# Optimization experiments

Hardware: AMD Instinct MI355X
Metric: run time of the kernel (lower is better)

## Reference

```python
import jax, jax.numpy as jnp
import numpy as np

D = 1024      # d_model
H = 16        # n_heads
DH = 64       # d_head
K = 4         # conv_kernel
C = H * DH    # channels for depthwise convs


def setup_inputs() -> dict:
    key = jax.random.key(0)
    ks = jax.random.split(key, 16)
    s = 0.02
    w = lambda k, shape: (jax.random.normal(k, shape, jnp.float32) * s)
    return {
        'hidden_states': jax.random.normal(ks[0], (4, 2048, D), jnp.float32),
        'Wq': w(ks[1], (C, D)),
        'Wk': w(ks[2], (C, D)),
        'Wv': w(ks[3], (C, D)),
        'Wa': w(ks[4], (H, D)), 'ba': jnp.zeros((H,), jnp.float32),
        'Wb': w(ks[5], (H, D)), 'bb': jnp.zeros((H,), jnp.float32),
        'conv_q_w': w(ks[6], (C, 1, K)), 'conv_q_b': jnp.zeros((C,), jnp.float32),
        'conv_k_w': w(ks[7], (C, 1, K)), 'conv_k_b': jnp.zeros((C,), jnp.float32),
        'conv_v_w': w(ks[8], (C, 1, K)), 'conv_v_b': jnp.zeros((C,), jnp.float32),
        'Wg': w(ks[9], (C, D)), 'bg': jnp.zeros((C,), jnp.float32),
        'Wo': w(ks[10], (D, C)),
    }


def _causal_conv(x, w, b):
    # x: (B, C, T); depthwise causal conv (torch pads K-1 both sides then slices [:T])
    y = jax.lax.conv_general_dilated(
        x, w, window_strides=(1,), padding=[(K - 1, 0)],
        feature_group_count=C, dimension_numbers=('NCH', 'OIH', 'NCH'))
    return y + b[None, :, None]


def reference(hidden_states, Wq, Wk, Wv, Wa, ba, Wb, bb,
              conv_q_w, conv_q_b, conv_k_w, conv_k_b, conv_v_w, conv_v_b,
              Wg, bg, Wo):
    B, T, _ = hidden_states.shape
    # projections -> (B, C, T) for conv
    q = jnp.einsum('btd,cd->bct', hidden_states, Wq)
    k = jnp.einsum('btd,cd->bct', hidden_states, Wk)
    v = jnp.einsum('btd,cd->bct', hidden_states, Wv)
    q = jax.nn.silu(_causal_conv(q, conv_q_w, conv_q_b))
    k = jax.nn.silu(_causal_conv(k, conv_k_w, conv_k_b))
    v = jax.nn.silu(_causal_conv(v, conv_v_w, conv_v_b))
    # (B, T, H, DH)
    q = q.transpose(0, 2, 1).reshape(B, T, H, DH)
    k = k.transpose(0, 2, 1).reshape(B, T, H, DH)
    v = v.transpose(0, 2, 1).reshape(B, T, H, DH)
    # F.normalize(k, p=2, dim=-1)
    k = k / jnp.maximum(jnp.linalg.norm(k, axis=-1, keepdims=True), 1e-12)
    alpha = jax.nn.sigmoid(jnp.einsum('btd,hd->bth', hidden_states, Wa) + ba)
    beta = jax.nn.sigmoid(jnp.einsum('btd,hd->bth', hidden_states, Wb) + bb)

    def step(S, xs):
        kt, vt, qt, at, bt = xs            # (B,H,DH) x3, (B,H) x2
        v_old = jnp.einsum('bhij,bhj->bhi', S, kt)
        upd = vt - at[..., None] * v_old   # (B,H,DH)
        dS = upd[..., :, None] * kt[..., None, :]
        S = jnp.clip(at[..., None, None] * S + bt[..., None, None] * dS, -5.0, 5.0)
        ot = jnp.einsum('bhij,bhj->bhi', S, qt)
        return S, ot

    S0 = jnp.zeros((B, H, DH, DH), hidden_states.dtype)
    xs = (k.transpose(1, 0, 2, 3), v.transpose(1, 0, 2, 3), q.transpose(1, 0, 2, 3),
          alpha.transpose(1, 0, 2), beta.transpose(1, 0, 2))
    _, ys = jax.lax.scan(step, S0, xs)     # ys: (T, B, H, DH)
    y = ys.transpose(1, 0, 2, 3).reshape(B, T, C)
    g = jax.nn.silu(jnp.einsum('btd,cd->btc', hidden_states, Wg) + bg)
    y = y * g
    out = jnp.einsum('btc,dc->btd', y, Wo)
    return out
```

## Files before the change

### kernel.cpp

```cpp
#include <hip/hip_runtime.h>
#include <cstdint>
#include <cstddef>

#define TSEQ 2048
#define NB   4
#define NH   16
#define MM   (NB * TSEQ)
#define KK   1024
#define NCAT 4224

typedef __attribute__((ext_vector_type(8))) __bf16 bf16x8;
typedef __attribute__((ext_vector_type(4))) float f32x4;
typedef __attribute__((ext_vector_type(4))) int   int4v;

__device__ __forceinline__ unsigned short f2bf(float f) {
  unsigned int u = __float_as_uint(f);
  u += 0x7fffu + ((u >> 16) & 1u);
  return (unsigned short)(u >> 16);
}
__device__ __forceinline__ float bf2f(unsigned short h) {
  return __uint_as_float(((unsigned int)h) << 16);
}
__device__ __forceinline__ float sigmoidf_(float x) { return 1.0f / (1.0f + expf(-x)); }
__device__ __forceinline__ float siluf_(float x)    { return x / (1.0f + expf(-x)); }

__device__ __forceinline__ uint32_t packsplit(float x) {
  unsigned short h = f2bf(x);
  unsigned short l = f2bf(x - bf2f(h));
  return ((uint32_t)h << 16) | (uint32_t)l;
}

union BF8 { bf16x8 v; unsigned short s[8]; };

__device__ __forceinline__ void frag_from_packed(const uint32_t* p, bf16x8& hi, bf16x8& lo) {
  int4v a = *(const int4v*)p;
  int4v b = *(const int4v*)(p + 4);
  BF8 H, L;
#pragma unroll
  for (int e = 0; e < 4; ++e) {
    uint32_t ua = ((const uint32_t*)&a)[e];
    uint32_t ub = ((const uint32_t*)&b)[e];
    H.s[e]     = (unsigned short)(ua >> 16);
    L.s[e]     = (unsigned short)(ua & 0xffffu);
    H.s[e + 4] = (unsigned short)(ub >> 16);
    L.s[e + 4] = (unsigned short)(ub & 0xffffu);
  }
  hi = H.v; lo = L.v;
}

__device__ __forceinline__ f32x4 mfma3(bf16x8 ah, bf16x8 al, bf16x8 bh, bf16x8 bl, f32x4 acc) {
  acc = __builtin_amdgcn_mfma_f32_16x16x32_bf16(ah, bh, acc, 0, 0, 0);
  acc = __builtin_amdgcn_mfma_f32_16x16x32_bf16(ah, bl, acc, 0, 0, 0);
  acc = __builtin_amdgcn_mfma_f32_16x16x32_bf16(al, bh, acc, 0, 0, 0);
  return acc;
}

__global__ void k_split(const float* __restrict__ x, unsigned short* __restrict__ hi,
                        unsigned short* __restrict__ lo, int n) {
  int idx = blockIdx.x * blockDim.x + threadIdx.x;
  if (idx >= n) return;
  float v = x[idx];
  unsigned short h = f2bf(v);
  hi[idx] = h;
  lo[idx] = f2bf(v - bf2f(h));
}

__global__ void k_build_wcat(const float* __restrict__ Wq, const float* __restrict__ Wk,
                             const float* __restrict__ Wv, const float* __restrict__ Wg,
                             const float* __restrict__ Wa, const float* __restrict__ Wb,
                             unsigned short* __restrict__ hi, unsigned short* __restrict__ lo) {
  int idx = blockIdx.x * blockDim.x + threadIdx.x;
  if (idx >= NCAT * KK) return;
  int row = idx >> 10, col = idx & 1023;
  float v = 0.0f;
  if      (row < 1024) v = Wq[idx];
  else if (row < 2048) v = Wk[idx - 1024 * 1024];
  else if (row < 3072) v = Wv[idx - 2048 * 1024];
  else if (row < 4096) v = Wg[idx - 3072 * 1024];
  else if (row < 4112) v = Wa[(row - 4096) * 1024 + col];
  else if (row < 4128) v = Wb[(row - 4112) * 1024 + col];
  unsigned short h = f2bf(v);
  hi[idx] = h;
  lo[idx] = f2bf(v - bf2f(h));
}

__global__ __launch_bounds__(256, 2)
void k_gemm(const unsigned short* __restrict__ Ahi, const unsigned short* __restrict__ Alo,
            const unsigned short* __restrict__ Bhi, const unsigned short* __restrict__ Blo,
            int Kdim, int mode,
            float* __restrict__ Qb, float* __restrict__ Kb, float* __restrict__ Vb,
            float* __restrict__ Gb, float* __restrict__ Ab, float* __restrict__ Bbuf,
            const float* __restrict__ bg, const float* __restrict__ ba, const float* __restrict__ bb,
            float* __restrict__ Out) {
  __shared__ __align__(16) unsigned short As_hi[128 * 32];
  __shared__ __align__(16) unsigned short As_lo[128 * 32];
  __shared__ __align__(16) unsigned short Bs_hi[128 * 32];
  __shared__ __align__(16) unsigned short Bs_lo[128 * 32];

  const int tid  = threadIdx.x;
  const int lane = tid & 63;
  const int l15  = lane & 15;
  const int quad = lane >> 4;
  const int wid  = tid >> 6;
  const int wm   = (wid >> 1) * 64;
  const int wn   = (wid & 1) * 64;
  const int m0   = blockIdx.x * 128;
  const int n0   = blockIdx.y * 128;
  const int srow = tid >> 2;
  const int skc  = (tid & 3) * 8;

  f32x4 acc[4][4];
  f32x4 zero4 = {0.f, 0.f, 0.f, 0.f};
#pragma unroll
  for (int i = 0; i < 4; ++i)
#pragma unroll
    for (int j = 0; j < 4; ++j) acc[i][j] = zero4;

  const unsigned short* pa0 = Ahi + (size_t)(m0 + srow) * Kdim + skc;
  const unsigned short* pa1 = Ahi + (size_t)(m0 + srow + 64) * Kdim + skc;
  const unsigned short* pa2 = Alo + (size_t)(m0 + srow) * Kdim + skc;
  const unsigned short* pa3 = Alo + (size_t)(m0 + srow + 64) * Kdim + skc;
  const unsigned short* pb0 = Bhi + (size_t)(n0 + srow) * Kdim + skc;
  const unsigned short* pb1 = Bhi + (size_t)(n0 + srow + 64) * Kdim + skc;
  const unsigned short* pb2 = Blo + (size_t)(n0 + srow) * Kdim + skc;
  const unsigned short* pb3 = Blo + (size_t)(n0 + srow + 64) * Kdim + skc;

  for (int kt = 0; kt < Kdim; kt += 32) {
    int4v va0 = *(const int4v*)(pa0 + kt);
    int4v va1 = *(const int4v*)(pa1 + kt);
    int4v va2 = *(const int4v*)(pa2 + kt);
    int4v va3 = *(const int4v*)(pa3 + kt);
    int4v vb0 = *(const int4v*)(pb0 + kt);
    int4v vb1 = *(const int4v*)(pb1 + kt);
    int4v vb2 = *(const int4v*)(pb2 + kt);
    int4v vb3 = *(const int4v*)(pb3 + kt);
    __syncthreads();
    *(int4v*)&As_hi[srow * 32 + skc]        = va0;
    *(int4v*)&As_hi[(srow + 64) * 32 + skc] = va1;
    *(int4v*)&As_lo[srow * 32 + skc]        = va2;
    *(int4v*)&As_lo[(srow + 64) * 32 + skc] = va3;
    *(int4v*)&Bs_hi[srow * 32 + skc]        = vb0;
    *(int4v*)&Bs_hi[(srow + 64) * 32 + skc] = vb1;
    *(int4v*)&Bs_lo[srow * 32 + skc]        = vb2;
    *(int4v*)&Bs_lo[(srow + 64) * 32 + skc] = vb3;
    __syncthreads();

    bf16x8 ah[4], al[4], bh[4], bl[4];
#pragma unroll
    for (int f = 0; f < 4; ++f) {
      int ra = (wm + f * 16 + l15) * 32 + quad * 8;
      ah[f] = *(const bf16x8*)&As_hi[ra];
      al[f] = *(const bf16x8*)&As_lo[ra];
      int rb = (wn + f * 16 + l15) * 32 + quad * 8;
      bh[f] = *(const bf16x8*)&Bs_hi[rb];
      bl[f] = *(const bf16x8*)&Bs_lo[rb];
    }
#pragma unroll
    for (int mf = 0; mf < 4; ++mf)
#pragma unroll
      for (int nf = 0; nf < 4; ++nf) {
        acc[mf][nf] = __builtin_amdgcn_mfma_f32_16x16x32_bf16(ah[mf], bh[nf], acc[mf][nf], 0, 0, 0);
        acc[mf][nf] = __builtin_amdgcn_mfma_f32_16x16x32_bf16(ah[mf], bl[nf], acc[mf][nf], 0, 0, 0);
        acc[mf][nf] = __builtin_amdgcn_mfma_f32_16x16x32_bf16(al[mf], bh[nf], acc[mf][nf], 0, 0, 0);
      }
  }

#pragma unroll
  for (int mf = 0; mf < 4; ++mf) {
    int rowb = m0 + wm + mf * 16 + quad * 4;
#pragma unroll
    for (int nf = 0; nf < 4; ++nf) {
      int col = n0 + wn + nf * 16 + l15;
      f32x4 v = acc[mf][nf];
      if (mode == 1) {
#pragma unroll
        for (int r = 0; r < 4; ++r) Out[(size_t)(rowb + r) * 1024 + col] = v[r];
      } else {
        if (col < 1024) {
#pragma unroll
          for (int r = 0; r < 4; ++r) Qb[(size_t)(rowb + r) * 1024 + col] = v[r];
        } else if (col < 2048) {
          int c = col - 1024;
#pragma unroll
          for (int r = 0; r < 4; ++r) Kb[(size_t)(rowb + r) * 1024 + c] = v[r];
        } else if (col < 3072) {
          int c = col - 2048;
#pragma unroll
          for (int r = 0; r < 4; ++r) Vb[(size_t)(rowb + r) * 1024 + c] = v[r];
        } else if (col < 4096) {
          int c = col - 3072;
          float bgc = bg[c];
#pragma unroll
          for (int r = 0; r < 4; ++r) {
            float x = v[r] + bgc;
            Gb[(size_t)(rowb + r) * 1024 + c] = siluf_(x);
          }
        } else if (col < 4112) {
          int c = col - 4096;
          float bac = ba[c];
#pragma unroll
          for (int r = 0; r < 4; ++r) Ab[(size_t)(rowb + r) * 16 + c] = sigmoidf_(v[r] + bac);
        } else if (col < 4128) {
          int c = col - 4112;
          float bbc = bb[c];
#pragma unroll
          for (int r = 0; r < 4; ++r) Bbuf[(size_t)(rowb + r) * 16 + c] = sigmoidf_(v[r] + bbc);
        }
      }
    }
  }
}

__global__ __launch_bounds__(512)
void k_intra(const float* __restrict__ Qb, const float* __restrict__ Kb,
             const float* __restrict__ Vb,
             const float* __restrict__ Ab, const float* __restrict__ Bb,
             const float* __restrict__ cqw, const float* __restrict__ cqb,
             const float* __restrict__ ckw, const float* __restrict__ ckb,
             const float* __restrict__ cvw, const float* __restrict__ cvb,
             uint32_t* __restrict__ A1buf, unsigned short* __restrict__ Qefbuf,
             unsigned short* __restrict__ G1buf, unsigned short* __restrict__ G2Tbuf,
             float* __restrict__ gCbuf) {
  __shared__ __align__(16) unsigned short Khi[64][72], Klo[64][72];
  __shared__ __align__(16) unsigned short Qhi[64][72], Qlo[64][72];
  __shared__ float Vf[64][65];
  __shared__ float Rf[64][65];
  __shared__ float Mm[64][68];
  __shared__ __align__(16) unsigned short Atthi[64][72];
  __shared__ __align__(16) uint32_t u0T[64][68], RTp[64][68];
  __shared__ __align__(16) unsigned short KwThi[64][72], KwTlo[64][72];
  __shared__ float lgs[64], gas[64], bss[64], wvs[64], ins[64];

  const int tid  = threadIdx.x;
  const int lane = tid & 63;
  const int w8   = tid >> 6;
  const int ws   = w8 & 3;
  const int hs   = w8 >> 2;
  const int l15  = lane & 15;
  const int quad = lane >> 4;
  const int bid  = blockIdx.x;
  const int c    = bid & 31;
  const int h    = (bid >> 5) & 15;
  const int b    = bid >> 9;
  const size_t ci = (size_t)bid;
  const int t0   = c * 64;
  const long rowBase = (long)b * 2048 + t0;
  const int ch   = h * 64 + lane;
  const f32x4 z4 = {0.f, 0.f, 0.f, 0.f};

  {
    long gr = (rowBase + lane) * 16 + h;
    float av = Ab[gr], bv = Bb[gr];
    float x = log2f(av);
#pragma unroll
    for (int off = 1; off < 64; off <<= 1) {
      float y = __shfl_up(x, off);
      if (lane >= off) x += y;
    }
    float l63 = __shfl(x, 63);
    lgs[lane] = x;
    gas[lane] = exp2f(x);
    bss[lane] = bv;
    wvs[lane] = exp2f(l63 - x) * bv;
  }

  {
    const float kc0 = ckw[ch * 4], kc1 = ckw[ch * 4 + 1], kc2 = ckw[ch * 4 + 2], kc3 = ckw[ch * 4 + 3], kcbv = ckb[ch];
    const float qc0 = cqw[ch * 4], qc1 = cqw[ch * 4 + 1], qc2 = cqw[ch * 4 + 2], qc3 = cqw[ch * 4 + 3], qcbv = cqb[ch];
    const float vc0 = cvw[ch * 4], vc1 = cvw[ch * 4 + 1], vc2 = cvw[ch * 4 + 2], vc3 = cvw[ch * 4 + 3], vcbv = cvb[ch];
    const int tb = t0 + w8 * 8;
    float kw0, kw1, kw2, qw0, qw1, qw2, vw0, vw1, vw2;
    {
      float kx[3], qx[3], vx[3];
#pragma unroll
      for (int d = 0; d < 3; ++d) {
        int tt = tb - 3 + d;
        float a = 0.f, bq = 0.f, cv = 0.f;
        if (tt >= 0) {
          long ro = ((long)b * 2048 + tt) * 1024 + ch;
          a = Kb[ro]; bq = Qb[ro]; cv = Vb[ro];
        }
        kx[d] = a; qx[d] = bq; vx[d] = cv;
      }
      kw0 = kx[0]; kw1 = kx[1]; kw2 = kx[2];
      qw0 = qx[0]; qw1 = qx[1]; qw2 = qx[2];
      vw0 = vx[0]; vw1 = vx[1]; vw2 = vx[2];
    }
#pragma unroll
    for (int lt = 0; lt < 8; ++lt) {
      const int s = w8 * 8 + lt;
      const long ro = (rowBase + s) * 1024 + ch;
      float kr = Kb[ro], qr = Qb[ro], vr = Vb[ro];
      float kcv = kcbv + kc0 * kw0 + kc1 * kw1 + kc2 * kw2 + kc3 * kr;
      float qcv = qcbv + qc0 * qw0 + qc1 * qw1 + qc2 * qw2 + qc3 * qr;
      float vcv = vcbv + vc0 * vw0 + vc1 * vw1 + vc2 * vw2 + vc3 * vr;
      kw0 = kw1; kw1 = kw2; kw2 = kr;
      qw0 = qw1; qw1 = qw2; qw2 = qr;
      vw0 = vw1; vw1 = vw2; vw2 = vr;
      float kv = siluf_(kcv), qv = siluf_(qcv), vv = siluf_(vcv);
      uint32_t kp_ = packsplit(kv);
      uint32_t qp_ = packsplit(qv);
      Khi[s][lane] = (unsigned short)(kp_ >> 16); Klo[s][lane] = (unsigned short)(kp_ & 0xffffu);
      Qhi[s][lane] = (unsigned short)(qp_ >> 16); Qlo[s][lane] = (unsigned short)(qp_ & 0xffffu);
      Vf[s][lane] = vv;
    }
  }
  __syncthreads();

  f32x4 accT[4];
#pragma unroll
  for (int nt = 0; nt < 4; ++nt) accT[nt] = z4;
#pragma unroll
  for (int ks = 0; ks < 2; ++ks) {
    bf16x8 ah, al;
    if (hs == 0) {
      ah = *(const bf16x8*)&Khi[ws * 16 + l15][ks * 32 + quad * 8];
      al = *(const bf16x8*)&Klo[ws * 16 + l15][ks * 32 + quad * 8];
    } else {
      ah = *(const bf16x8*)&Qhi[ws * 16 + l15][ks * 32 + quad * 8];
      al = *(const bf16x8*)&Qlo[ws * 16 + l15][ks * 32 + quad * 8];
    }
#pragma unroll
    for (int nt = 0; nt < 4; ++nt) {
      bf16x8 bh = *(const bf16x8*)&Khi[nt * 16 + l15][ks * 32 + quad * 8];
      bf16x8 bl = *(const bf16x8*)&Klo[nt * 16 + l15][ks * 32 + quad * 8];
      accT[nt] = mfma3(ah, al, bh, bl, accT[nt]);
    }
  }
  if (hs == 0) {
#pragma unroll
    for (int nt = 0; nt < 4; ++nt)
      if (nt == ws) {
#pragma unroll
        for (int r = 0; r < 4; ++r)
          if (l15 == quad * 4 + r) ins[nt * 16 + l15] = rsqrtf(fmaxf(accT[nt][r], 1e-24f));
      }
  }
  __syncthreads();

  {
    if (hs == 0) {
#pragma unroll
      for (int nt = 0; nt < 4; ++nt) {
        int sc = nt * 16 + l15;
        float insc = ins[sc], lgc = lgs[sc], bsc = bss[sc];
#pragma unroll
        for (int r = 0; r < 4; ++r) {
          int sr = ws * 16 + quad * 4 + r;
          Mm[sr][sc] = (sc < sr) ? exp2f(lgs[sr] - lgc) * bsc * ins[sr] * insc * accT[nt][r] : 0.f;
        }
      }
    } else {
#pragma unroll
      for (int nt = 0; nt < 4; ++nt) {
        int sc = nt * 16 + l15;
        float insc = ins[sc], lgc = lgs[sc], bsc = bss[sc];
#pragma unroll
        for (int r = 0; r < 4; ++r) {
          int sr = ws * 16 + quad * 4 + r;
          Atthi[sr][sc] = f2bf((sc <= sr) ? exp2f(lgs[sr] - lgc) * bsc * insc * accT[nt][r] : 0.f);
        }
      }
    }
    int s = w8 * 8 + (lane & 7);
    int jb = (lane >> 3) * 8;
    float rsc = gas[s] * ins[s];
    float wsc = wvs[s] * ins[s];
    BF8 H0, L0;
    H0.v = *(const bf16x8*)&Khi[s][jb];
    L0.v = *(const bf16x8*)&Klo[s][jb];
#pragma unroll
    for (int e = 0; e < 8; ++e) {
      float kv = bf2f(H0.s[e]) + bf2f(L0.s[e]);
      Rf[s][jb + e] = kv * rsc;
      uint32_t p0 = packsplit(kv * wsc);
      KwThi[jb + e][s] = (unsigned short)(p0 >> 16);
      KwTlo[jb + e][s] = (unsigned short)(p0 & 0xffffu);
    }
  }
  if (tid == 0) gCbuf[ci] = gas[63];
  __syncthreads();

  if (w8 < 2) {
    float* RHS = (w8 == 0) ? &Vf[0][0] : &Rf[0][0];
    const int i = lane;
    float u[64];
#pragma unroll
    for (int d = 0; d < 4; ++d) {
      const int base = d * 16;
#pragma unroll
      for (int r2 = 0; r2 < 16; ++r2) {
        const int s = base + r2;
        float acc = RHS[s * 65 + i];
#pragma unroll
        for (int r = 0; r < r2; ++r) acc = fmaf(-Mm[s][base + r], u[base + r], acc);
        u[s] = acc;
        RHS[s * 65 + i] = acc;
      }
      if (d < 3) {
#pragma unroll 1
        for (int s = base + 16; s < 64; ++s) {
          f32x4 m0 = *(const f32x4*)&Mm[s][base];
          f32x4 m1 = *(const f32x4*)&Mm[s][base + 4];
          f32x4 m2 = *(const f32x4*)&Mm[s][base + 8];
          f32x4 m3 = *(const f32x4*)&Mm[s][base + 12];
          float a0 = m0[0] * u[base + 0] + m0[1] * u[base + 1] + m0[2] * u[base + 2] + m0[3] * u[base + 3];
          float a1 = m1[0] * u[base + 4] + m1[1] * u[base + 5] + m1[2] * u[base + 6] + m1[3] * u[base + 7];
          float a2 = m2[0] * u[base + 8] + m2[1] * u[base + 9] + m2[2] * u[base + 10] + m2[3] * u[base + 11];
          float a3 = m3[0] * u[base + 12] + m3[1] * u[base + 13] + m3[2] * u[base + 14] + m3[3] * u[base + 15];
          RHS[s * 65 + i] = RHS[s * 65 + i] - ((a0 + a1) + (a2 + a3));
        }
      }
    }
  }
  __syncthreads();

#pragma unroll
  for (int r = 0; r < 8; ++r) {
    int i = w8 * 8 + r;
    u0T[i][lane] = packsplit(Vf[lane][i]);
    RTp[i][lane] = packsplit(Rf[lane][i]);
  }
  __syncthreads();

  if (hs == 0) {
    {
      f32x4 acc[4];
#pragma unroll
      for (int nt = 0; nt < 4; ++nt) acc[nt] = z4;
#pragma unroll
      for (int ks = 0; ks < 2; ++ks) {
        bf16x8 ta = *(const bf16x8*)&Atthi[ws * 16 + l15][ks * 32 + quad * 8];
#pragma unroll
        for (int nt = 0; nt < 4; ++nt) {
          bf16x8 uh, ul;
          frag_from_packed(&u0T[nt * 16 + l15][ks * 32 + quad * 8], uh, ul);
          acc[nt] = __builtin_amdgcn_mfma_f32_16x16x32_bf16(ta, uh, acc[nt], 0, 0, 0);
          acc[nt] = __builtin_amdgcn_mfma_f32_16x16x32_bf16(ta, ul, acc[nt], 0, 0, 0);
        }
      }
#pragma unroll
      for (int nt = 0; nt < 4; ++nt)
#pragma unroll
        for (int r = 0; r < 4; ++r) {
          int t = ws * 16 + quad * 4 + r, i = nt * 16 + l15;
          A1buf[ci * 4096 + t * 64 + i] = packsplit(acc[nt][r]);
        }
    }
    {
      f32x4 acc[4];
#pragma unroll
      for (int nt = 0; nt < 4; ++nt) acc[nt] = z4;
#pragma unroll
      for (int ks = 0; ks < 2; ++ks) {
        bf16x8 ta = *(const bf16x8*)&Atthi[ws * 16 + l15][ks * 32 + quad * 8];
#pragma unroll
        for (int nt = 0; nt < 4; ++nt) {
          bf16x8 rh, rl;
          frag_from_packed(&RTp[nt * 16 + l15][ks * 32 + quad * 8], rh, rl);
          acc[nt] = __builtin_amdgcn_mfma_f32_16x16x32_bf16(ta, rh, acc[nt], 0, 0, 0);
          acc[nt] = __builtin_amdgcn_mfma_f32_16x16x32_bf16(ta, rl, acc[nt], 0, 0, 0);
        }
      }
#pragma unroll
      for (int nt = 0; nt < 4; ++nt)
#pragma unroll
        for (int r = 0; r < 4; ++r) {
          int t = ws * 16 + quad * 4 + r, j = nt * 16 + l15;
          float q = bf2f(Qhi[t][j]) + bf2f(Qlo[t][j]);
          Qefbuf[ci * 4096 + t * 64 + j] = f2bf(gas[t] * q - acc[nt][r]);
        }
    }
  } else {
    {
      f32x4 acc[4];
#pragma unroll
      for (int nt = 0; nt < 4; ++nt) acc[nt] = z4;
#pragma unroll
      for (int ks = 0; ks < 2; ++ks) {
        bf16x8 uh, ul;
        frag_from_packed(&u0T[ws * 16 + l15][ks * 32 + quad * 8], uh, ul);
#pragma unroll
        for (int nt = 0; nt < 4; ++nt) {
          bf16x8 kh = *(const bf16x8*)&KwThi[nt * 16 + l15][ks * 32 + quad * 8];
          bf16x8 kl = *(const bf16x8*)&KwTlo[nt * 16 + l15][ks * 32 + quad * 8];
          acc[nt] = mfma3(uh, ul, kh, kl, acc[nt]);
        }
      }
#pragma unroll
      for (int nt = 0; nt < 4; ++nt)
#pragma unroll
        for (int r = 0; r < 4; ++r) {
          int i = ws * 16 + quad * 4 + r, j = nt * 16 + l15;
          G1buf[ci * 4096 + i * 64 + j] = f2bf(acc[nt][r]);
        }
    }
    {
      f32x4 acc[4];
#pragma unroll
      for (int nt = 0; nt < 4; ++nt) acc[nt] = z4;
#pragma unroll
      for (int ks = 0; ks < 2; ++ks) {
        bf16x8 rh, rl;
        frag_from_packed(&RTp[ws * 16 + l15][ks * 32 + quad * 8], rh, rl);
#pragma unroll
        for (int nt = 0; nt < 4; ++nt) {
          bf16x8 kh = *(const bf16x8*)&KwThi[nt * 16 + l15][ks * 32 + quad * 8];
          bf16x8 kl = *(const bf16x8*)&KwTlo[nt * 16 + l15][ks * 32 + quad * 8];
          acc[nt] = mfma3(rh, rl, kh, kl, acc[nt]);
        }
      }
#pragma unroll
      for (int nt = 0; nt < 4; ++nt) {
        int j = nt * 16 + l15;
        int mb = ws * 16 + quad * 4;
        uint32_t lo32 = (uint32_t)f2bf(acc[nt][0]) | ((uint32_t)f2bf(acc[nt][1]) << 16);
        uint32_t hi32 = (uint32_t)f2bf(acc[nt][2]) | ((uint32_t)f2bf(acc[nt][3]) << 16);
        uint32_t* dst = (uint32_t*)&G2Tbuf[ci * 4096 + j * 64 + mb];
        dst[0] = lo32; dst[1] = hi32;
      }
    }
  }
}

__global__ __launch_bounds__(256)
void k_serial(const uint32_t* __restrict__ A1buf, const unsigned short* __restrict__ Qefbuf,
              const unsigned short* __restrict__ G1buf, const unsigned short* __restrict__ G2Tbuf,
              const float* __restrict__ gCbuf, const float* __restrict__ Gb,
              unsigned short* __restrict__ Yhi, unsigned short* __restrict__ Ylo) {
  __shared__ uint32_t A1L[64][66];
  __shared__ __align__(16) unsigned short QefL[64][72], G1L[64][72], G2TL[64][72];
  __shared__ __align__(16) unsigned short S0hi[64][72], S0lo[64][72];
  __shared__ float S0f[64][65];

  const int tid  = threadIdx.x;
  const int lane = tid & 63;
  const int w    = tid >> 6;
  const int l15  = lane & 15;
  const int quad = lane >> 4;
  const int b    = blockIdx.x >> 4;
  const int h    = blockIdx.x & 15;
  const size_t bh = (size_t)blockIdx.x;
  const f32x4 z4 = {0.f, 0.f, 0.f, 0.f};

  for (int n = tid; n < 64 * 65; n += 256) (&S0f[0][0])[n] = 0.f;
  for (int n = tid; n < 64 * 72; n += 256) { (&S0hi[0][0])[n] = 0; (&S0lo[0][0])[n] = 0; }

  uint32_t rA[16], rQ[8], rG1[8], rG2[8];
  float pg[16], pgC;
  {
    const uint32_t* pA = A1buf + bh * 32 * 4096;
    const uint32_t* pQ = (const uint32_t*)Qefbuf + bh * 32 * 2048;
    const uint32_t* pG1 = (const uint32_t*)G1buf + bh * 32 * 2048;
    const uint32_t* pG2 = (const uint32_t*)G2Tbuf + bh * 32 * 2048;
#pragma unroll
    for (int k = 0; k < 16; ++k) rA[k] = pA[tid + k * 256];
#pragma unroll
    for (int k = 0; k < 8; ++k) { rQ[k] = pQ[tid + k * 256]; rG1[k] = pG1[tid + k * 256]; rG2[k] = pG2[tid + k * 256]; }
    pgC = gCbuf[bh * 32];
#pragma unroll
    for (int nt = 0; nt < 4; ++nt)
#pragma unroll
      for (int r = 0; r < 4; ++r)
        pg[nt * 4 + r] = Gb[((long)b * 2048 + w * 16 + quad * 4 + r) * 1024 + h * 64 + nt * 16 + l15];
  }
  __syncthreads();

#pragma unroll 1
  for (int c = 0; c < 32; ++c) {
#pragma unroll
    for (int k = 0; k < 16; ++k) {
      int idx = tid + k * 256;
      A1L[idx >> 6][idx & 63] = rA[k];
    }
#pragma unroll
    for (int k = 0; k < 8; ++k) {
      int i32 = tid + k * 256;
      int row = i32 >> 5, col = (i32 & 31) * 2;
      *(uint32_t*)&QefL[row][col] = rQ[k];
      *(uint32_t*)&G1L[row][col]  = rG1[k];
      *(uint32_t*)&G2TL[row][col] = rG2[k];
    }
    float gC = pgC;
    float pgl[16];
#pragma unroll
    for (int e = 0; e < 16; ++e) pgl[e] = pg[e];
    __syncthreads();

    f32x4 accO[4], accS[4];
#pragma unroll
    for (int nt = 0; nt < 4; ++nt) { accO[nt] = z4; accS[nt] = z4; }
#pragma unroll
    for (int ks = 0; ks < 2; ++ks) {
      bf16x8 qa = *(const bf16x8*)&QefL[w * 16 + l15][ks * 32 + quad * 8];
      bf16x8 sah = *(const bf16x8*)&S0hi[w * 16 + l15][ks * 32 + quad * 8];
      bf16x8 sal = *(const bf16x8*)&S0lo[w * 16 + l15][ks * 32 + quad * 8];
#pragma unroll
      for (int nt = 0; nt < 4; ++nt) {
        bf16x8 sh = *(const bf16x8*)&S0hi[nt * 16 + l15][ks * 32 + quad * 8];
        bf16x8 sl = *(const bf16x8*)&S0lo[nt * 16 + l15][ks * 32 + quad * 8];
        accO[nt] = __builtin_amdgcn_mfma_f32_16x16x32_bf16(qa, sh, accO[nt], 0, 0, 0);
        accO[nt] = __builtin_amdgcn_mfma_f32_16x16x32_bf16(qa, sl, accO[nt], 0, 0, 0);
        bf16x8 g2 = *(const bf16x8*)&G2TL[nt * 16 + l15][ks * 32 + quad * 8];
        accS[nt] = __builtin_amdgcn_mfma_f32_16x16x32_bf16(sah, g2, accS[nt], 0, 0, 0);
        accS[nt] = __builtin_amdgcn_mfma_f32_16x16x32_bf16(sal, g2, accS[nt], 0, 0, 0);
      }
    }
    {
      const int cc = (c + 1 < 32) ? c + 1 : 31;
      const uint32_t* pA = A1buf + (bh * 32 + cc) * 4096;
      const uint32_t* pQ = (const uint32_t*)Qefbuf + (bh * 32 + cc) * 2048;
      const uint32_t* pG1 = (const uint32_t*)G1buf + (bh * 32 + cc) * 2048;
      const uint32_t* pG2 = (const uint32_t*)G2Tbuf + (bh * 32 + cc) * 2048;
#pragma unroll
      for (int k = 0; k < 16; ++k) rA[k] = pA[tid + k * 256];
#pragma unroll
      for (int k = 0; k < 8; ++k) { rQ[k] = pQ[tid + k * 256]; rG1[k] = pG1[tid + k * 256]; rG2[k] = pG2[tid + k * 256]; }
      pgC = gCbuf[bh * 32 + cc];
#pragma unroll
      for (int nt = 0; nt < 4; ++nt)
#pragma unroll
        for (int r = 0; r < 4; ++r)
          pg[nt * 4 + r] = Gb[((long)b * 2048 + cc * 64 + w * 16 + quad * 4 + r) * 1024 + h * 64 + nt * 16 + l15];
    }
    __syncthreads();

#pragma unroll
    for (int nt = 0; nt < 4; ++nt)
#pragma unroll
      for (int r = 0; r < 4; ++r) {
        int t = w * 16 + quad * 4 + r, i = nt * 16 + l15;
        uint32_t a1 = A1L[t][i];
        float o = accO[nt][r] + bf2f((unsigned short)(a1 >> 16)) + bf2f((unsigned short)(a1 & 0xffffu));
        float y = o * pgl[nt * 4 + r];
        long ro = ((long)b * 2048 + c * 64 + t) * 1024 + h * 64 + i;
        unsigned short hy = f2bf(y);
        Yhi[ro] = hy;
        Ylo[ro] = f2bf(y - bf2f(hy));
      }
#pragma unroll
    for (int nt = 0; nt < 4; ++nt)
#pragma unroll
      for (int r = 0; r < 4; ++r) {
        int i = w * 16 + quad * 4 + r, j = nt * 16 + l15;
        float sn = gC * S0f[i][j] + bf2f(G1L[i][j]) - accS[nt][r];
        S0f[i][j] = sn;
        uint32_t p = packsplit(sn);
        S0hi[i][j] = (unsigned short)(p >> 16);
        S0lo[i][j] = (unsigned short)(p & 0xffffu);
      }
    __syncthreads();
  }
}

extern "C" void kernel_launch(void* const* d_in, const int* in_sizes, int n_in,
                              void* d_out, int out_size, void* d_ws, size_t ws_size,
                              hipStream_t stream) {
  const float* X   = (const float*)d_in[0];
  const float* Wq  = (const float*)d_in[1];
  const float* Wk  = (const float*)d_in[2];
  const float* Wv  = (const float*)d_in[3];
  const float* Wa  = (const float*)d_in[4];
  const float* ba  = (const float*)d_in[5];
  const float* Wb  = (const float*)d_in[6];
  const float* bb  = (const float*)d_in[7];
  const float* cqw = (const float*)d_in[8];
  const float* cqb = (const float*)d_in[9];
  const float* ckw = (const float*)d_in[10];
  const float* ckb = (const float*)d_in[11];
  const float* cvw = (const float*)d_in[12];
  const float* cvb = (const float*)d_in[13];
  const float* Wg  = (const float*)d_in[14];
  const float* bg  = (const float*)d_in[15];
  const float* Wo  = (const float*)d_in[16];
  float* Out = (float*)d_out;

  char* ws = (char*)d_ws;
  size_t off = 0;
  auto alloc = [&](size_t bytes) -> void* {
    void* p = ws + off;
    off += (bytes + 255) & ~(size_t)255;
    return p;
  };
  unsigned short* Xhi = (unsigned short*)alloc((size_t)MM * KK * 2);
  unsigned short* Xlo = (unsigned short*)alloc((size_t)MM * KK * 2);
  unsigned short* Whi = (unsigned short*)alloc((size_t)NCAT * KK * 2);
  unsigned short* Wlo = (unsigned short*)alloc((size_t)NCAT * KK * 2);
  float* Qb  = (float*)alloc((size_t)MM * 1024 * 4);
  float* Kb  = (float*)alloc((size_t)MM * 1024 * 4);
  float* Vb  = (float*)alloc((size_t)MM * 1024 * 4);
  float* Ab  = (float*)alloc((size_t)MM * 16 * 4);
  float* Bbf = (float*)alloc((size_t)MM * 16 * 4);
  uint32_t*       A1buf  = (uint32_t*)alloc((size_t)2048 * 4096 * 4);
  unsigned short* G1buf  = (unsigned short*)alloc((size_t)2048 * 4096 * 2);
  unsigned short* G2Tbuf = (unsigned short*)alloc((size_t)2048 * 4096 * 2);
  float*          gCbuf  = (float*)alloc((size_t)2048 * 4);
  float* Gb = Out;
  unsigned short* Yhi = Xhi;
  unsigned short* Ylo = Xlo;
  unsigned short* Qefbuf = Whi;
  unsigned short* Wohi = Whi;
  unsigned short* Wolo = Wlo;

  const int nX = MM * KK;
  k_split<<<(nX + 255) / 256, 256, 0, stream>>>(X, Xhi, Xlo, nX);
  k_build_wcat<<<(NCAT * KK + 255) / 256, 256, 0, stream>>>(Wq, Wk, Wv, Wg, Wa, Wb, Whi, Wlo);
  k_gemm<<<dim3(MM / 128, NCAT / 128), 256, 0, stream>>>(
      Xhi, Xlo, Whi, Wlo, KK, 0, Qb, Kb, Vb, Gb, Ab, Bbf, bg, ba, bb, nullptr);
  k_intra<<<NB * NH * 32, 512, 0, stream>>>(Qb, Kb, Vb, Ab, Bbf,
                                            cqw, cqb, ckw, ckb, cvw, cvb,
                                            A1buf, Qefbuf, G1buf, G2Tbuf, gCbuf);
  k_serial<<<NB * NH, 256, 0, stream>>>(A1buf, Qefbuf, G1buf, G2Tbuf, gCbuf, Gb, Yhi, Ylo);
  k_split<<<(1024 * 1024 + 255) / 256, 256, 0, stream>>>(Wo, Wohi, Wolo, 1024 * 1024);
  k_gemm<<<dim3(MM / 128, 1024 / 128), 256, 0, stream>>>(
      Yhi, Ylo, Wohi, Wolo, KK, 1, nullptr, nullptr, nullptr, nullptr, nullptr, nullptr,
      nullptr, nullptr, nullptr, Out);
}
```

Baseline: 703.0 us.

## Rewrite split-bf16 GEMM with 256x256 tiles, async LDS loads and double buffering

Replaces the 128x128 GEMM tile with a 256x256 tile across 8 waves. Global loads go straight into LDS with global_load_lds, using an XOR swizzle and double-buffered stages that are interleaved with MFMA quads under raised priority. The three hi/lo cross terms become three K segments, 48 steps of 64, each with its own operand pair, instead of three MFMAs per fragment. The weight concat is padded to a multiple of 256, adding wasted rows and higher register and LDS pressure in exchange for better reuse and latency hiding.

Measured after the change: 886.2 us. +26.1%, slower.

```diff
diff --git a/kernel.cpp b/kernel.cpp
--- a/kernel.cpp
+++ b/kernel.cpp
@@ -7,11 +7,14 @@
 #define NH   16
 #define MM   (NB * TSEQ)
 #define KK   1024
-#define NCAT 4224
+#define NPAD 4352
 
 typedef __attribute__((ext_vector_type(8))) __bf16 bf16x8;
 typedef __attribute__((ext_vector_type(4))) float f32x4;
 typedef __attribute__((ext_vector_type(4))) int   int4v;
+
+typedef __attribute__((address_space(3))) unsigned char lds_uc;
+typedef __attribute__((address_space(1))) unsigned char glb_uc;
 
 __device__ __forceinline__ unsigned short f2bf(float f) {
   unsigned int u = __float_as_uint(f);
@@ -70,7 +73,7 @@
                              const float* __restrict__ Wa, const float* __restrict__ Wb,
                              unsigned short* __restrict__ hi, unsigned short* __restrict__ lo) {
   int idx = blockIdx.x * blockDim.x + threadIdx.x;
-  if (idx >= NCAT * KK) return;
+  if (idx >= NPAD * KK) return;
   int row = idx >> 10, col = idx & 1023;
   float v = 0.0f;
   if      (row < 1024) v = Wq[idx];
@@ -84,89 +87,114 @@
   lo[idx] = f2bf(v - bf2f(h));
 }
 
-__global__ __launch_bounds__(256, 2)
+__device__ __forceinline__ void stage_half(unsigned short* region, const unsigned short* src,
+                                           int row0, int k0, int half, int tid) {
+#pragma unroll
+  for (int sub = 0; sub < 2; ++sub) {
+    int L = half * 16384 + sub * 8192 + tid * 16;
+    int P = L ^ (((L >> 7) & 7) << 4);
+    int r = P >> 7;
+    int c = (P & 127) >> 1;
+    const unsigned short* g = src + (size_t)(row0 + r) * KK + (k0 + c);
+    unsigned short* l = region + (half * 8192 + sub * 4096 + ((tid >> 6) << 9));
+    __builtin_amdgcn_global_load_lds((const glb_uc*)g, (lds_uc*)l, 16, 0, 0);
+  }
+}
+
+#define LOAD_A(mh) \
+  _Pragma("unroll") for (int mi = 0; mi < 4; ++mi) \
+  _Pragma("unroll") for (int ks = 0; ks < 2; ++ks) \
+    Afr[mi][ks] = *(const bf16x8*)((const unsigned char*)Ac + ((wm + (mh)*64 + mi*16 + l15) << 7) + ((((ks)*4 + quad) << 4) ^ xorv));
+
+#define LOAD_B(np) \
+  _Pragma("unroll") for (int ni = 0; ni < 2; ++ni) \
+  _Pragma("unroll") for (int ks = 0; ks < 2; ++ks) \
+    Bfr[ni][ks] = *(const bf16x8*)((const unsigned char*)Bc + ((wn + (np)*32 + ni*16 + l15) << 7) + ((((ks)*4 + quad) << 4) ^ xorv));
+
+#define QUAD(mh, np) \
+  __builtin_amdgcn_s_setprio(1); \
+  _Pragma("unroll") for (int mi = 0; mi < 4; ++mi) \
+  _Pragma("unroll") for (int ni = 0; ni < 2; ++ni) \
+  _Pragma("unroll") for (int ks = 0; ks < 2; ++ks) \
+    acc[(mh)*4 + mi][(np)*2 + ni] = __builtin_amdgcn_mfma_f32_16x16x32_bf16( \
+        Afr[mi][ks], Bfr[ni][ks], acc[(mh)*4 + mi][(np)*2 + ni], 0, 0, 0); \
+  __builtin_amdgcn_s_setprio(0);
+
+__global__ __launch_bounds__(512, 2)
 void k_gemm(const unsigned short* __restrict__ Ahi, const unsigned short* __restrict__ Alo,
             const unsigned short* __restrict__ Bhi, const unsigned short* __restrict__ Blo,
-            int Kdim, int mode,
+            int mode,
             float* __restrict__ Qb, float* __restrict__ Kb, float* __restrict__ Vb,
             float* __restrict__ Gb, float* __restrict__ Ab, float* __restrict__ Bbuf,
             const float* __restrict__ bg, const float* __restrict__ ba, const float* __restrict__ bb,
             float* __restrict__ Out) {
-  __shared__ __align__(16) unsigned short As_hi[128 * 32];
-  __shared__ __align__(16) unsigned short As_lo[128 * 32];
-  __shared__ __align__(16) unsigned short Bs_hi[128 * 32];
-  __shared__ __align__(16) unsigned short Bs_lo[128 * 32];
+  __shared__ __align__(1024) unsigned short Asm_[2][16384];
+  __shared__ __align__(1024) unsigned short Bsm_[2][16384];
 
   const int tid  = threadIdx.x;
   const int lane = tid & 63;
   const int l15  = lane & 15;
   const int quad = lane >> 4;
-  const int wid  = tid >> 6;
-  const int wm   = (wid >> 1) * 64;
-  const int wn   = (wid & 1) * 64;
-  const int m0   = blockIdx.x * 128;
-  const int n0   = blockIdx.y * 128;
-  const int srow = tid >> 2;
-  const int skc  = (tid & 3) * 8;
-
-  f32x4 acc[4][4];
-  f32x4 zero4 = {0.f, 0.f, 0.f, 0.f};
-#pragma unroll
-  for (int i = 0; i < 4; ++i)
-#pragma unroll
-    for (int j = 0; j < 4; ++j) acc[i][j] = zero4;
-
-  const unsigned short* pa0 = Ahi + (size_t)(m0 + srow) * Kdim + skc;
-  const unsigned short* pa1 = Ahi + (size_t)(m0 + srow + 64) * Kdim + skc;
-  const unsigned short* pa2 = Alo + (size_t)(m0 + srow) * Kdim + skc;
-  const unsigned short* pa3 = Alo + (size_t)(m0 + srow + 64) * Kdim + skc;
-  const unsigned short* pb0 = Bhi + (size_t)(n0 + srow) * Kdim + skc;
-  const unsigned short* pb1 = Bhi + (size_t)(n0 + srow + 64) * Kdim + skc;
-  const unsigned short* pb2 = Blo + (size_t)(n0 + srow) * Kdim + skc;
-  const unsigned short* pb3 = Blo + (size_t)(n0 + srow + 64) * Kdim + skc;
-
-  for (int kt = 0; kt < Kdim; kt += 32) {
-    int4v va0 = *(const int4v*)(pa0 + kt);
-    int4v va1 = *(const int4v*)(pa1 + kt);
-    int4v va2 = *(const int4v*)(pa2 + kt);
-    int4v va3 = *(const int4v*)(pa3 + kt);
-    int4v vb0 = *(const int4v*)(pb0 + kt);
-    int4v vb1 = *(const int4v*)(pb1 + kt);
-    int4v vb2 = *(const int4v*)(pb2 + kt);
-    int4v vb3 = *(const int4v*)(pb3 + kt);
-    __syncthreads();
-    *(int4v*)&As_hi[srow * 32 + skc]        = va0;
-    *(int4v*)&As_hi[(srow + 64) * 32 + skc] = va1;
-    *(int4v*)&As_lo[srow * 32 + skc]        = va2;
-    *(int4v*)&As_lo[(srow + 64) * 32 + skc] = va3;
-    *(int4v*)&Bs_hi[srow * 32 + skc]        = vb0;
-    *(int4v*)&Bs_hi[(srow + 64) * 32 + skc] = vb1;
-    *(int4v*)&Bs_lo[srow * 32 + skc]        = vb2;
-    *(int4v*)&Bs_lo[(srow + 64) * 32 + skc] = vb3;
-    __syncthreads();
-
-    bf16x8 ah[4], al[4], bh[4], bl[4];
-#pragma unroll
-    for (int f = 0; f < 4; ++f) {
-      int ra = (wm + f * 16 + l15) * 32 + quad * 8;
-      ah[f] = *(const bf16x8*)&As_hi[ra];
-      al[f] = *(const bf16x8*)&As_lo[ra];
-      int rb = (wn + f * 16 + l15) * 32 + quad * 8;
-      bh[f] = *(const bf16x8*)&Bs_hi[rb];
-      bl[f] = *(const bf16x8*)&Bs_lo[rb];
-    }
-#pragma unroll
-    for (int mf = 0; mf < 4; ++mf)
-#pragma unroll
-      for (int nf = 0; nf < 4; ++nf) {
-        acc[mf][nf] = __builtin_amdgcn_mfma_f32_16x16x32_bf16(ah[mf], bh[nf], acc[mf][nf], 0, 0, 0);
-        acc[mf][nf] = __builtin_amdgcn_mfma_f32_16x16x32_bf16(ah[mf], bl[nf], acc[mf][nf], 0, 0, 0);
-        acc[mf][nf] = __builtin_amdgcn_mfma_f32_16x16x32_bf16(al[mf], bh[nf], acc[mf][nf], 0, 0, 0);
-      }
-  }
-
-#pragma unroll
-  for (int mf = 0; mf < 4; ++mf) {
+  const int w8   = tid >> 6;
+  const int wm   = (w8 >> 2) * 128;
+  const int wn   = (w8 & 3) * 64;
+  const int m0   = blockIdx.x * 256;
+  const int n0   = blockIdx.y * 256;
+  const int xorv = (l15 & 7) << 4;
+
+  f32x4 acc[8][4];
+  f32x4 z4 = {0.f, 0.f, 0.f, 0.f};
+#pragma unroll
+  for (int i = 0; i < 8; ++i)
+#pragma unroll
+    for (int j = 0; j < 4; ++j) acc[i][j] = z4;
+
+  stage_half(&Asm_[0][0], Ahi, m0, 0, 0, tid);
+  stage_half(&Asm_[0][0], Ahi, m0, 0, 1, tid);
+  stage_half(&Bsm_[0][0], Bhi, n0, 0, 0, tid);
+  stage_half(&Bsm_[0][0], Bhi, n0, 0, 1, tid);
+
+#pragma unroll 1
+  for (int t = 0; t < 48; ++t) {
+    const int buf = t & 1;
+    unsigned short* Ac = &Asm_[buf][0];
+    unsigned short* Bc = &Bsm_[buf][0];
+    unsigned short* An = &Asm_[buf ^ 1][0];
+    unsigned short* Bn = &Bsm_[buf ^ 1][0];
+    const bool havep = (t + 1) < 48;
+    const int tn = havep ? (t + 1) : 0;
+    const int seg = tn >> 4;
+    const unsigned short* sA = (seg == 2) ? Alo : Ahi;
+    const unsigned short* sB = (seg == 1) ? Blo : Bhi;
+    const int k1 = (tn & 15) << 6;
+
+    asm volatile("" ::: "memory");
+    __builtin_amdgcn_s_barrier();
+    asm volatile("" ::: "memory");
+    if (havep) stage_half(An, sA, m0, k1, 0, tid);
+    if (havep) { asm volatile("s_waitcnt vmcnt(2)" ::: "memory"); }
+    else       { asm volatile("s_waitcnt vmcnt(0)" ::: "memory"); }
+    __builtin_amdgcn_s_barrier();
+    asm volatile("" ::: "memory");
+    __builtin_amdgcn_sched_barrier(0);
+
+    bf16x8 Afr[4][2], Bfr[2][2];
+    LOAD_A(0)
+    LOAD_B(0)
+    QUAD(0, 0)
+    if (havep) stage_half(An, sA, m0, k1, 1, tid);
+    LOAD_B(1)
+    QUAD(0, 1)
+    if (havep) stage_half(Bn, sB, n0, k1, 0, tid);
+    LOAD_A(1)
+    QUAD(1, 1)
+    if (havep) stage_half(Bn, sB, n0, k1, 1, tid);
+    LOAD_B(0)
+    QUAD(1, 0)
+  }
+
+#pragma unroll
+  for (int mf = 0; mf < 8; ++mf) {
     int rowb = m0 + wm + mf * 16 + quad * 4;
 #pragma unroll
     for (int nf = 0; nf < 4; ++nf) {
@@ -684,8 +712,8 @@
   };
   unsigned short* Xhi = (unsigned short*)alloc((size_t)MM * KK * 2);
   unsigned short* Xlo = (unsigned short*)alloc((size_t)MM * KK * 2);
-  unsigned short* Whi = (unsigned short*)alloc((size_t)NCAT * KK * 2);
-  unsigned short* Wlo = (unsigned short*)alloc((size_t)NCAT * KK * 2);
+  unsigned short* Whi = (unsigned short*)alloc((size_t)NPAD * KK * 2);
+  unsigned short* Wlo = (unsigned short*)alloc((size_t)NPAD * KK * 2);
   float* Qb  = (float*)alloc((size_t)MM * 1024 * 4);
   float* Kb  = (float*)alloc((size_t)MM * 1024 * 4);
   float* Vb  = (float*)alloc((size_t)MM * 1024 * 4);
@@ -704,15 +732,15 @@
 
   const int nX = MM * KK;
   k_split<<<(nX + 255) / 256, 256, 0, stream>>>(X, Xhi, Xlo, nX);
-  k_build_wcat<<<(NCAT * KK + 255) / 256, 256, 0, stream>>>(Wq, Wk, Wv, Wg, Wa, Wb, Whi, Wlo);
-  k_gemm<<<dim3(MM / 128, NCAT / 128), 256, 0, stream>>>(
-      Xhi, Xlo, Whi, Wlo, KK, 0, Qb, Kb, Vb, Gb, Ab, Bbf, bg, ba, bb, nullptr);
+  k_build_wcat<<<(NPAD * KK + 255) / 256, 256, 0, stream>>>(Wq, Wk, Wv, Wg, Wa, Wb, Whi, Wlo);
+  k_gemm<<<dim3(MM / 256, NPAD / 256), 512, 0, stream>>>(
+      Xhi, Xlo, Whi, Wlo, 0, Qb, Kb, Vb, Gb, Ab, Bbf, bg, ba, bb, nullptr);
   k_intra<<<NB * NH * 32, 512, 0, stream>>>(Qb, Kb, Vb, Ab, Bbf,
                                             cqw, cqb, ckw, ckb, cvw, cvb,
                                             A1buf, Qefbuf, G1buf, G2Tbuf, gCbuf);
   k_serial<<<NB * NH, 256, 0, stream>>>(A1buf, Qefbuf, G1buf, G2Tbuf, gCbuf, Gb, Yhi, Ylo);
   k_split<<<(1024 * 1024 + 255) / 256, 256, 0, stream>>>(Wo, Wohi, Wolo, 1024 * 1024);
-  k_gemm<<<dim3(MM / 128, 1024 / 128), 256, 0, stream>>>(
-      Yhi, Ylo, Wohi, Wolo, KK, 1, nullptr, nullptr, nullptr, nullptr, nullptr, nullptr,
+  k_gemm<<<dim3(MM / 256, 1024 / 256), 512, 0, stream>>>(
+      Yhi, Ylo, Wohi, Wolo, 1, nullptr, nullptr, nullptr, nullptr, nullptr, nullptr,
       nullptr, nullptr, nullptr, Out);
 }
```

## Split serial chunk recurrence across four blocks by state row quarter

Applied to the files above, without the earlier changes.

The serial inter-chunk recurrence kernel now launches four blocks per (batch, head), each owning 16 rows of the 64x64 state. Rows of the state evolve independently given the per-chunk factors, so each block keeps only its slice of S and computes its quarter of the output columns. This raises the grid from 64 to 256 blocks to fill more compute units and cuts per-block MFMA and shared-memory work. In exchange, Q and G2T chunk data are loaded redundantly by all four blocks.

After: 647.3 us. 1.09x faster.

```diff
diff --git a/kernel.cpp b/kernel.cpp
--- a/kernel.cpp
+++ b/kernel.cpp
@@ -528,127 +528,121 @@
               const unsigned short* __restrict__ G1buf, const unsigned short* __restrict__ G2Tbuf,
               const float* __restrict__ gCbuf, const float* __restrict__ Gb,
               unsigned short* __restrict__ Yhi, unsigned short* __restrict__ Ylo) {
-  __shared__ uint32_t A1L[64][66];
-  __shared__ __align__(16) unsigned short QefL[64][72], G1L[64][72], G2TL[64][72];
-  __shared__ __align__(16) unsigned short S0hi[64][72], S0lo[64][72];
-  __shared__ float S0f[64][65];
+  __shared__ uint32_t A1L[64][18];
+  __shared__ __align__(16) unsigned short QefL[64][72], G2TL[64][72];
+  __shared__ __align__(16) unsigned short G1L[16][72];
+  __shared__ __align__(16) unsigned short S0hi[16][72], S0lo[16][72];
+  __shared__ float S0f[16][65];
 
   const int tid  = threadIdx.x;
   const int lane = tid & 63;
   const int w    = tid >> 6;
   const int l15  = lane & 15;
   const int quad = lane >> 4;
-  const int b    = blockIdx.x >> 4;
-  const int h    = blockIdx.x & 15;
-  const size_t bh = (size_t)blockIdx.x;
+  const int bh   = blockIdx.x >> 2;
+  const int iq   = blockIdx.x & 3;
+  const int ibase = iq * 16;
+  const int b    = bh >> 4;
+  const int h    = bh & 15;
   const f32x4 z4 = {0.f, 0.f, 0.f, 0.f};
 
-  for (int n = tid; n < 64 * 65; n += 256) (&S0f[0][0])[n] = 0.f;
-  for (int n = tid; n < 64 * 72; n += 256) { (&S0hi[0][0])[n] = 0; (&S0lo[0][0])[n] = 0; }
-
-  uint32_t rA[16], rQ[8], rG1[8], rG2[8];
-  float pg[16], pgC;
+  for (int n = tid; n < 16 * 65; n += 256) (&S0f[0][0])[n] = 0.f;
+  for (int n = tid; n < 16 * 72; n += 256) { (&S0hi[0][0])[n] = 0; (&S0lo[0][0])[n] = 0; }
+
+  uint32_t rA[4], rQ[8], rG1[2], rG2[8];
+  float pg[4], pgC;
   {
-    const uint32_t* pA = A1buf + bh * 32 * 4096;
-    const uint32_t* pQ = (const uint32_t*)Qefbuf + bh * 32 * 2048;
-    const uint32_t* pG1 = (const uint32_t*)G1buf + bh * 32 * 2048;
-    const uint32_t* pG2 = (const uint32_t*)G2Tbuf + bh * 32 * 2048;
-#pragma unroll
-    for (int k = 0; k < 16; ++k) rA[k] = pA[tid + k * 256];
-#pragma unroll
-    for (int k = 0; k < 8; ++k) { rQ[k] = pQ[tid + k * 256]; rG1[k] = pG1[tid + k * 256]; rG2[k] = pG2[tid + k * 256]; }
-    pgC = gCbuf[bh * 32];
-#pragma unroll
-    for (int nt = 0; nt < 4; ++nt)
-#pragma unroll
-      for (int r = 0; r < 4; ++r)
-        pg[nt * 4 + r] = Gb[((long)b * 2048 + w * 16 + quad * 4 + r) * 1024 + h * 64 + nt * 16 + l15];
+    const uint32_t* pA  = A1buf + (size_t)bh * 32 * 4096;
+    const uint32_t* pQ  = (const uint32_t*)Qefbuf + (size_t)bh * 32 * 2048;
+    const uint32_t* pG1 = (const uint32_t*)G1buf  + (size_t)bh * 32 * 2048;
+    const uint32_t* pG2 = (const uint32_t*)G2Tbuf + (size_t)bh * 32 * 2048;
+#pragma unroll
+    for (int k = 0; k < 4; ++k) { int idx = tid + k * 256; rA[k] = pA[(idx >> 4) * 64 + ibase + (idx & 15)]; }
+#pragma unroll
+    for (int k = 0; k < 8; ++k) { rQ[k] = pQ[tid + k * 256]; rG2[k] = pG2[tid + k * 256]; }
+#pragma unroll
+    for (int k = 0; k < 2; ++k) { int idx = tid + k * 256; rG1[k] = pG1[(ibase + (idx >> 5)) * 32 + (idx & 31)]; }
+    pgC = gCbuf[(size_t)bh * 32];
+#pragma unroll
+    for (int r = 0; r < 4; ++r)
+      pg[r] = Gb[((long)b * 2048 + w * 16 + quad * 4 + r) * 1024 + h * 64 + ibase + l15];
   }
   __syncthreads();
 
 #pragma unroll 1
   for (int c = 0; c < 32; ++c) {
 #pragma unroll
-    for (int k = 0; k < 16; ++k) {
-      int idx = tid + k * 256;
-      A1L[idx >> 6][idx & 63] = rA[k];
-    }
+    for (int k = 0; k < 4; ++k) { int idx = tid + k * 256; A1L[idx >> 4][idx & 15] = rA[k]; }
 #pragma unroll
     for (int k = 0; k < 8; ++k) {
       int i32 = tid + k * 256;
       int row = i32 >> 5, col = (i32 & 31) * 2;
       *(uint32_t*)&QefL[row][col] = rQ[k];
-      *(uint32_t*)&G1L[row][col]  = rG1[k];
       *(uint32_t*)&G2TL[row][col] = rG2[k];
     }
+#pragma unroll
+    for (int k = 0; k < 2; ++k) {
+      int i32 = tid + k * 256;
+      int row = i32 >> 5, col = (i32 & 31) * 2;
+      *(uint32_t*)&G1L[row][col] = rG1[k];
+    }
     float gC = pgC;
-    float pgl[16];
-#pragma unroll
-    for (int e = 0; e < 16; ++e) pgl[e] = pg[e];
+    float pgl[4];
+#pragma unroll
+    for (int e = 0; e < 4; ++e) pgl[e] = pg[e];
     __syncthreads();
 
-    f32x4 accO[4], accS[4];
-#pragma unroll
-    for (int nt = 0; nt < 4; ++nt) { accO[nt] = z4; accS[nt] = z4; }
+    f32x4 accO = z4, accS = z4;
 #pragma unroll
     for (int ks = 0; ks < 2; ++ks) {
-      bf16x8 qa = *(const bf16x8*)&QefL[w * 16 + l15][ks * 32 + quad * 8];
-      bf16x8 sah = *(const bf16x8*)&S0hi[w * 16 + l15][ks * 32 + quad * 8];
-      bf16x8 sal = *(const bf16x8*)&S0lo[w * 16 + l15][ks * 32 + quad * 8];
-#pragma unroll
-      for (int nt = 0; nt < 4; ++nt) {
-        bf16x8 sh = *(const bf16x8*)&S0hi[nt * 16 + l15][ks * 32 + quad * 8];
-        bf16x8 sl = *(const bf16x8*)&S0lo[nt * 16 + l15][ks * 32 + quad * 8];
-        accO[nt] = __builtin_amdgcn_mfma_f32_16x16x32_bf16(qa, sh, accO[nt], 0, 0, 0);
-        accO[nt] = __builtin_amdgcn_mfma_f32_16x16x32_bf16(qa, sl, accO[nt], 0, 0, 0);
-        bf16x8 g2 = *(const bf16x8*)&G2TL[nt * 16 + l15][ks * 32 + quad * 8];
-        accS[nt] = __builtin_amdgcn_mfma_f32_16x16x32_bf16(sah, g2, accS[nt], 0, 0, 0);
-        accS[nt] = __builtin_amdgcn_mfma_f32_16x16x32_bf16(sal, g2, accS[nt], 0, 0, 0);
-      }
+      bf16x8 qa  = *(const bf16x8*)&QefL[w * 16 + l15][ks * 32 + quad * 8];
+      bf16x8 sh0 = *(const bf16x8*)&S0hi[l15][ks * 32 + quad * 8];
+      bf16x8 sl0 = *(const bf16x8*)&S0lo[l15][ks * 32 + quad * 8];
+      accO = __builtin_amdgcn_mfma_f32_16x16x32_bf16(qa, sh0, accO, 0, 0, 0);
+      accO = __builtin_amdgcn_mfma_f32_16x16x32_bf16(qa, sl0, accO, 0, 0, 0);
+      bf16x8 g2 = *(const bf16x8*)&G2TL[w * 16 + l15][ks * 32 + quad * 8];
+      accS = __builtin_amdgcn_mfma_f32_16x16x32_bf16(sh0, g2, accS, 0, 0, 0);
+      accS = __builtin_amdgcn_mfma_f32_16x16x32_bf16(sl0, g2, accS, 0, 0, 0);
     }
     {
       const int cc = (c + 1 < 32) ? c + 1 : 31;
-      const uint32_t* pA = A1buf + (bh * 32 + cc) * 4096;
-      const uint32_t* pQ = (const uint32_t*)Qefbuf + (bh * 32 + cc) * 2048;
-      const uint32_t* pG1 = (const uint32_t*)G1buf + (bh * 32 + cc) * 2048;
-      const uint32_t* pG2 = (const uint32_t*)G2Tbuf + (bh * 32 + cc) * 2048;
-#pragma unroll
-      for (int k = 0; k < 16; ++k) rA[k] = pA[tid + k * 256];
-#pragma unroll
-      for (int k = 0; k < 8; ++k) { rQ[k] = pQ[tid + k * 256]; rG1[k] = pG1[tid + k * 256]; rG2[k] = pG2[tid + k * 256]; }
-      pgC = gCbuf[bh * 32 + cc];
-#pragma unroll
-      for (int nt = 0; nt < 4; ++nt)
-#pragma unroll
-        for (int r = 0; r < 4; ++r)
-          pg[nt * 4 + r] = Gb[((long)b * 2048 + cc * 64 + w * 16 + quad * 4 + r) * 1024 + h * 64 + nt * 16 + l15];
+      const uint32_t* pA  = A1buf + ((size_t)bh * 32 + cc) * 4096;
+      const uint32_t* pQ  = (const uint32_t*)Qefbuf + ((size_t)bh * 32 + cc) * 2048;
+      const uint32_t* pG1 = (const uint32_t*)G1buf  + ((size_t)bh * 32 + cc) * 2048;
+      const uint32_t* pG2 = (const uint32_t*)G2Tbuf + ((size_t)bh * 32 + cc) * 2048;
+#pragma unroll
+      for (int k = 0; k < 4; ++k) { int idx = tid + k * 256; rA[k] = pA[(idx >> 4) * 64 + ibase + (idx & 15)]; }
+#pragma unroll
+      for (int k = 0; k < 8; ++k) { rQ[k] = pQ[tid + k * 256]; rG2[k] = pG2[tid + k * 256]; }
+#pragma unroll
+      for (int k = 0; k < 2; ++k) { int idx = tid + k * 256; rG1[k] = pG1[(ibase + (idx >> 5)) * 32 + (idx & 31)]; }
+      pgC = gCbuf[(size_t)bh * 32 + cc];
+#pragma unroll
+      for (int r = 0; r < 4; ++r)
+        pg[r] = Gb[((long)b * 2048 + cc * 64 + w * 16 + quad * 4 + r) * 1024 + h * 64 + ibase + l15];
     }
     __syncthreads();
 
 #pragma unroll
-    for (int nt = 0; nt < 4; ++nt)
-#pragma unroll
-      for (int r = 0; r < 4; ++r) {
-        int t = w * 16 + quad * 4 + r, i = nt * 16 + l15;
-        uint32_t a1 = A1L[t][i];
-        float o = accO[nt][r] + bf2f((unsigned short)(a1 >> 16)) + bf2f((unsigned short)(a1 & 0xffffu));
-        float y = o * pgl[nt * 4 + r];
-        long ro = ((long)b * 2048 + c * 64 + t) * 1024 + h * 64 + i;
-        unsigned short hy = f2bf(y);
-        Yhi[ro] = hy;
-        Ylo[ro] = f2bf(y - bf2f(hy));
-      }
-#pragma unroll
-    for (int nt = 0; nt < 4; ++nt)
-#pragma unroll
-      for (int r = 0; r < 4; ++r) {
-        int i = w * 16 + quad * 4 + r, j = nt * 16 + l15;
-        float sn = gC * S0f[i][j] + bf2f(G1L[i][j]) - accS[nt][r];
-        S0f[i][j] = sn;
-        uint32_t p = packsplit(sn);
-        S0hi[i][j] = (unsigned short)(p >> 16);
-        S0lo[i][j] = (unsigned short)(p & 0xffffu);
-      }
+    for (int r = 0; r < 4; ++r) {
+      int t = w * 16 + quad * 4 + r;
+      uint32_t a1 = A1L[t][l15];
+      float o = accO[r] + bf2f((unsigned short)(a1 >> 16)) + bf2f((unsigned short)(a1 & 0xffffu));
+      float y = o * pgl[r];
+      long ro = ((long)b * 2048 + c * 64 + t) * 1024 + h * 64 + ibase + l15;
+      unsigned short hy = f2bf(y);
+      Yhi[ro] = hy;
+      Ylo[ro] = f2bf(y - bf2f(hy));
+    }
+#pragma unroll
+    for (int r = 0; r < 4; ++r) {
+      int i = quad * 4 + r, j = w * 16 + l15;
+      float sn = gC * S0f[i][j] + bf2f(G1L[i][j]) - accS[r];
+      S0f[i][j] = sn;
+      uint32_t p = packsplit(sn);
+      S0hi[i][j] = (unsigned short)(p >> 16);
+      S0lo[i][j] = (unsigned short)(p & 0xffffu);
+    }
     __syncthreads();
   }
 }
@@ -710,7 +704,7 @@
   k_intra<<<NB * NH * 32, 512, 0, stream>>>(Qb, Kb, Vb, Ab, Bbf,
                                             cqw, cqb, ckw, ckb, cvw, cvb,
                                             A1buf, Qefbuf, G1buf, G2Tbuf, gCbuf);
-  k_serial<<<NB * NH, 256, 0, stream>>>(A1buf, Qefbuf, G1buf, G2Tbuf, gCbuf, Gb, Yhi, Ylo);
+  k_serial<<<NB * NH * 4, 256, 0, stream>>>(A1buf, Qefbuf, G1buf, G2Tbuf, gCbuf, Gb, Yhi, Ylo);
   k_split<<<(1024 * 1024 + 255) / 256, 256, 0, stream>>>(Wo, Wohi, Wolo, 1024 * 1024);
   k_gemm<<<dim3(MM / 128, 1024 / 128), 256, 0, stream>>>(
       Yhi, Ylo, Wohi, Wolo, KK, 1, nullptr, nullptr, nullptr, nullptr, nullptr, nullptr,
```
